# Kernel optimization log

Hardware: AMD Instinct MI355X
Metric: run time of the kernel (lower is better)

## Reference

```python
import jax, jax.numpy as jnp
import numpy as np

B, S, F, D = 64, 129, 768, 4
MOM = 0.9
EPS = 1e-6


def setup_inputs() -> dict:
    key = jax.random.key(0)
    ks = jax.random.split(key, 8)
    x = jax.random.normal(ks[0], (B, S, F), dtype=jnp.float32)
    labels = jax.random.randint(ks[1], (B,), 0, 16, dtype=jnp.int32)
    domain = jax.random.randint(ks[2], (B,), 0, D, dtype=jnp.int32)
    lmda = jax.random.beta(ks[3], 0.1, 0.1, (B, 1, 1)).astype(jnp.float32)
    d_rand = jax.random.randint(ks[4], (B,), 1, D, dtype=jnp.int32)  # range(1, num_domains)
    mean_buf = (0.1 * jax.random.normal(ks[5], (D, F))).astype(jnp.float32)
    var_buf = jax.random.uniform(ks[6], (D, F), minval=0.5, maxval=1.5, dtype=jnp.float32)
    hg_noise = jax.random.normal(ks[7], (B, S, F), dtype=jnp.float32)
    return {"input": x, "lmda": lmda, "mean_buf": mean_buf, "var_buf": var_buf,
            "hg_noise": hg_noise, "labels": labels, "domain": domain, "d_rand": d_rand}


def reference(input, lmda, mean_buf, var_buf, hg_noise, labels, domain, d_rand):
    x = input  # [B,S,F]
    b, s, f = x.shape
    d = mean_buf.shape[0]

    # --- per-domain mean/var over dims [0,1] (unbiased), momentum buffer update ---
    tok = x.reshape(b * s, f)
    seg = jnp.repeat(domain, s)  # [B*S]
    cnt = jax.ops.segment_sum(jnp.ones((b * s,), x.dtype), seg, num_segments=d)  # tokens/domain
    s1 = jax.ops.segment_sum(tok, seg, num_segments=d)          # [D,F]
    s2 = jax.ops.segment_sum(tok * tok, seg, num_segments=d)    # [D,F]
    n = cnt[:, None]
    mu_d = s1 / jnp.maximum(n, 1.0)
    var_d = (s2 - n * mu_d * mu_d) / jnp.maximum(n - 1.0, 1.0)  # unbiased, matches torch.var
    present = (cnt > 0)[:, None]
    new_mean = jnp.where(present, MOM * mean_buf + (1.0 - MOM) * mu_d, mean_buf)
    new_var = jnp.where(present, MOM * var_buf + (1.0 - MOM) * var_d, var_buf)

    # --- instance renorm over token dim (unbiased var) + cross-domain restyle ---
    mu_i = x.mean(1, keepdims=True)
    v_i = x.var(1, keepdims=True, ddof=1)
    x_normed = (x - mu_i) * jax.lax.rsqrt(v_i + EPS)
    ds = (domain + d_rand) % d
    x_new = x_normed * jnp.sqrt(new_var[ds] + EPS)[:, None, :] + new_mean[ds][:, None, :]
    x_mix = lmda * x + (1.0 - lmda) * x_new

    # --- Gaussian hallucinated samples from own-domain stats ---
    hg = new_mean[domain][:, None, :] + jnp.sqrt(new_var[domain] + EPS)[:, None, :] * hg_noise

    # --- pairwise euclidean distance + hard example mining + soft-margin triplet loss ---
    xe = jnp.concatenate([x, x_mix, hg], axis=0).reshape(3 * b, s * f)  # [3B, S*F]
    ln = jnp.concatenate([labels, labels, -jnp.ones((b,), labels.dtype)])
    sq = jnp.sum(xe * xe, axis=1)
    d2 = sq[:, None] + sq[None, :] - 2.0 * (xe @ xe.T)
    dist = jnp.sqrt(jnp.clip(d2, 1e-12))
    pos = ln[:, None] == ln[None, :]
    big = jnp.asarray(1e30, dist.dtype)
    dist_ap = jnp.max(jnp.where(pos, dist, -big), axis=1)
    dist_an = jnp.min(jnp.where(pos, big, dist), axis=1)
    tri_hard_loss = jnp.mean(jax.nn.softplus(dist_ap - dist_an))  # SoftMarginLoss, y=1

    return x_mix, tri_hard_loss, new_mean, new_var
```

## Files before the change

### kernel.cpp

```cpp
#include <hip/hip_runtime.h>
#include <math.h>

#define B_ 64
#define S_ 129
#define F_ 768
#define N3 192
#define BF 49152
#define NCHUNK 1548
#define GMAIN 256
#define GSZ 36864

#define WS_NM   0
#define WS_SV   3072
#define WS_C1   6144
#define WS_C0   55296
#define WS_HGM  104448
#define WS_HGS  153600
#define WS_S1   202752
#define WS_S2   251904
#define WS_PART 337920

#define OUT_LOSS 6340608
#define OUT_NM   6340609
#define OUT_NV   6343681

typedef unsigned int uint;
using short8v = __attribute__((ext_vector_type(8))) short;
using float4v = __attribute__((ext_vector_type(4))) float;

__global__ void k_stats(const float* __restrict__ x,
                        float* __restrict__ s1, float* __restrict__ s2) {
    __shared__ float4 r1[256], r2[256];
    int b = blockIdx.x / 3, fg = blockIdx.x % 3;
    int c = threadIdx.x & 63, sp = threadIdx.x >> 6;
    int f = fg * 256 + c * 4;
    const float* p = x + (size_t)b * S_ * F_ + f;
    int s0 = sp * 32;
    int se = s0 + 32 + (sp == 3 ? 1 : 0);
    float4 a1 = {0.f,0.f,0.f,0.f}, a2 = {0.f,0.f,0.f,0.f};
#pragma unroll 4
    for (int s = s0; s < se; ++s) {
        float4 v = *(const float4*)(p + s * F_);
        a1.x += v.x; a1.y += v.y; a1.z += v.z; a1.w += v.w;
        a2.x += v.x*v.x; a2.y += v.y*v.y; a2.z += v.z*v.z; a2.w += v.w*v.w;
    }
    r1[threadIdx.x] = a1; r2[threadIdx.x] = a2;
    __syncthreads();
    if (sp == 0) {
        float4 t1 = r1[c], t2 = r2[c];
#pragma unroll
        for (int k = 1; k < 4; ++k) {
            float4 u1 = r1[k * 64 + c], u2 = r2[k * 64 + c];
            t1.x += u1.x; t1.y += u1.y; t1.z += u1.z; t1.w += u1.w;
            t2.x += u2.x; t2.y += u2.y; t2.z += u2.z; t2.w += u2.w;
        }
        *(float4*)(s1 + b * F_ + f) = t1;
        *(float4*)(s2 + b * F_ + f) = t2;
    }
}

__global__ void k_dom(const float* __restrict__ s1, const float* __restrict__ s2,
                      const int* __restrict__ domain,
                      const float* __restrict__ mean_buf, const float* __restrict__ var_buf,
                      float* __restrict__ nm_tab, float* __restrict__ sv_tab,
                      float* __restrict__ out_nm, float* __restrict__ out_nv) {
    int idx = blockIdx.x * 256 + threadIdx.x;
    if (idx >= F_ * 4) return;
    int f = idx >> 2, d = idx & 3;
    float a1 = 0.f, a2 = 0.f, cntf = 0.f;
#pragma unroll 8
    for (int b = 0; b < B_; ++b) {
        float v1 = s1[b * F_ + f];
        float v2 = s2[b * F_ + f];
        bool mk = (domain[b] == d);
        a1 += mk ? v1 : 0.0f;
        a2 += mk ? v2 : 0.0f;
        cntf += mk ? 1.0f : 0.0f;
    }
    float nm, nv;
    if (cntf > 0.f) {
        float n = cntf * (float)S_;
        float mu = a1 / n;
        float var = (a2 - n * mu * mu) / fmaxf(n - 1.0f, 1.0f);
        nm = 0.9f * mean_buf[d * F_ + f] + 0.1f * mu;
        nv = 0.9f * var_buf[d * F_ + f] + 0.1f * var;
    } else {
        nm = mean_buf[d * F_ + f];
        nv = var_buf[d * F_ + f];
    }
    out_nm[d * F_ + f] = nm;
    out_nv[d * F_ + f] = nv;
    nm_tab[d * F_ + f] = nm;
    sv_tab[d * F_ + f] = sqrtf(nv + 1e-6f);
}

__global__ void k_coef(const float* __restrict__ s1, const float* __restrict__ s2,
                       const float* __restrict__ lmda,
                       const int* __restrict__ domain, const int* __restrict__ d_rand,
                       const float* __restrict__ nm_tab, const float* __restrict__ sv_tab,
                       float* __restrict__ c1, float* __restrict__ c0,
                       float* __restrict__ hgm, float* __restrict__ hgs,
                       float* __restrict__ out_loss) {
    int t = blockIdx.x * 256 + threadIdx.x;
    if (blockIdx.x == 0 && threadIdx.x == 0) out_loss[0] = 0.0f;
    int b = t / F_, f = t - b * F_;
    float mu = s1[t] * (1.0f / (float)S_);
    float v  = (s2[t] - (float)S_ * mu * mu) * (1.0f / (float)(S_ - 1));
    float r  = rsqrtf(v + 1e-6f);
    int dm = domain[b];
    int ds = (dm + d_rand[b]) & 3;
    float sv = sv_tab[ds * F_ + f];
    float nm = nm_tab[ds * F_ + f];
    float lam = lmda[b];
    float rs = r * sv;
    c1[t] = lam + (1.0f - lam) * rs;
    c0[t] = (1.0f - lam) * (nm - mu * rs);
    hgm[t] = nm_tab[dm * F_ + f];
    hgs[t] = sv_tab[dm * F_ + f];
}

__device__ __forceinline__ uint pack2(float a, float b) {
    uint ua = __float_as_uint(a);
    uint ub = __float_as_uint(b);
    uint ha = (ua + 0x7FFFu + ((ua >> 16) & 1u)) >> 16;
    uint hb = (ub + 0x7FFFu + ((ub >> 16) & 1u)) & 0xFFFF0000u;
    return hb | ha;
}

__device__ __forceinline__ void bf16_store8(char* lds, int row, int g,
                                            float4 v0, float4 v1) {
    uint4 H;
    H.x = pack2(v0.x, v0.y);
    H.y = pack2(v0.z, v0.w);
    H.z = pack2(v1.x, v1.y);
    H.w = pack2(v1.z, v1.w);
    *(uint4*)(lds + row * 128 + ((g ^ (row & 7)) << 4)) = H;
}

__device__ __forceinline__ float4 fma4(float4 a, float4 x, float4 b) {
    float4 r;
    r.x = fmaf(a.x, x.x, b.x); r.y = fmaf(a.y, x.y, b.y);
    r.z = fmaf(a.z, x.z, b.z); r.w = fmaf(a.w, x.w, b.w);
    return r;
}

template <bool EXCL>
__global__ __launch_bounds__(512, 2)
void k_main(const float* __restrict__ x, const float* __restrict__ hgn,
            const float* __restrict__ c1, const float* __restrict__ c0,
            const float* __restrict__ hgm, const float* __restrict__ hgs,
            float* __restrict__ xmix, float* part, int npart) {
    __shared__ __align__(16) char LDS[49152];
    float4v acc[6][3];
#pragma unroll
    for (int i = 0; i < 6; ++i)
#pragma unroll
        for (int j = 0; j < 3; ++j)
            acc[i][j] = (float4v){0.f, 0.f, 0.f, 0.f};

    int tid = threadIdx.x;
    int b = tid >> 3;
    int g = tid & 7;
    int w = tid >> 6;
    int wr = (w >> 2) * 96, wc = (w & 3) * 48;
    int lane = tid & 63, m = lane & 15, qd = lane >> 4;

    int q = blockIdx.x;
    size_t goff; int cb;
    {
        int s = q / 12, f0 = (q - s * 12) * 64;
        goff = ((size_t)b * S_ + s) * F_ + f0 + (g << 3);
        cb = b * F_ + f0 + (g << 3);
    }
    float4 X0 = ((const float4*)(x + goff))[0];
    float4 X1 = ((const float4*)(x + goff))[1];
    float4 N0 = ((const float4*)(hgn + goff))[0];
    float4 N1 = ((const float4*)(hgn + goff))[1];
    float4 C1a = ((const float4*)(c1 + cb))[0], C1b = ((const float4*)(c1 + cb))[1];
    float4 C0a = ((const float4*)(c0 + cb))[0], C0b = ((const float4*)(c0 + cb))[1];
    float4 HMa = ((const float4*)(hgm + cb))[0], HMb = ((const float4*)(hgm + cb))[1];
    float4 HSa = ((const float4*)(hgs + cb))[0], HSb = ((const float4*)(hgs + cb))[1];

    int par = 0;
    for (; q < NCHUNK; q += GMAIN) {
        char* buf = LDS + par * 24576;
        float4 M0 = fma4(C1a, X0, C0a);
        float4 M1 = fma4(C1b, X1, C0b);
        ((float4*)(xmix + goff))[0] = M0;
        ((float4*)(xmix + goff))[1] = M1;
        float4 H0 = fma4(HSa, N0, HMa);
        float4 H1 = fma4(HSb, N1, HMb);

        bf16_store8(buf, b, g, X0, X1);
        bf16_store8(buf, 64 + b, g, M0, M1);
        bf16_store8(buf, 128 + b, g, H0, H1);
        __syncthreads();

        int qn = q + GMAIN;
        if (qn < NCHUNK) {
            int s = qn / 12, f0 = (qn - s * 12) * 64;
            goff = ((size_t)b * S_ + s) * F_ + f0 + (g << 3);
            cb = b * F_ + f0 + (g << 3);
            X0 = ((const float4*)(x + goff))[0];
            X1 = ((const float4*)(x + goff))[1];
            N0 = ((const float4*)(hgn + goff))[0];
            N1 = ((const float4*)(hgn + goff))[1];
            C1a = ((const float4*)(c1 + cb))[0]; C1b = ((const float4*)(c1 + cb))[1];
            C0a = ((const float4*)(c0 + cb))[0]; C0b = ((const float4*)(c0 + cb))[1];
            HMa = ((const float4*)(hgm + cb))[0]; HMb = ((const float4*)(hgm + cb))[1];
            HSa = ((const float4*)(hgs + cb))[0]; HSb = ((const float4*)(hgs + cb))[1];
        }

#pragma unroll
        for (int t = 0; t < 2; ++t) {
            short8v A[6];
#pragma unroll
            for (int i = 0; i < 6; ++i) {
                int row = wr + i * 16 + m;
                int go = (((t << 2) + qd) ^ (row & 7)) << 4;
                A[i] = *(const short8v*)(buf + row * 128 + go);
            }
#pragma unroll
            for (int j = 0; j < 3; ++j) {
                int row = wc + j * 16 + m;
                int go = (((t << 2) + qd) ^ (row & 7)) << 4;
                short8v Bv = *(const short8v*)(buf + row * 128 + go);
#pragma unroll
                for (int i = 0; i < 6; ++i)
                    acc[i][j] = __builtin_amdgcn_mfma_f32_16x16x32_bf16(A[i], Bv, acc[i][j], 0, 0, 0);
            }
        }
        par ^= 1;
    }

    float* dst = part + (size_t)(blockIdx.x % npart) * GSZ;
#pragma unroll
    for (int i = 0; i < 6; ++i)
#pragma unroll
        for (int j = 0; j < 3; ++j) {
            int base = (wr + i * 16 + qd * 4) * N3 + wc + j * 16 + m;
#pragma unroll
            for (int r = 0; r < 4; ++r) {
                int o = base + r * N3;
                if (EXCL) dst[o] = acc[i][j][r];
                else atomicAdd(dst + o, acc[i][j][r]);
            }
        }
}

__global__ void k_red(const float* __restrict__ part, float* __restrict__ gram, int npart) {
    int j = blockIdx.x * 256 + threadIdx.x;
    float s = 0.0f;
#pragma unroll 8
    for (int p = 0; p < npart; ++p) s += part[(size_t)p * GSZ + j];
    gram[j] = s;
}

__global__ void k_loss(const float* __restrict__ gram, const int* __restrict__ labels,
                       float* __restrict__ out_loss) {
    __shared__ float sq[N3];
    __shared__ int ln[N3];
    int i = blockIdx.x, lane = threadIdx.x;
    for (int k = lane; k < N3; k += 64) {
        sq[k] = gram[k * (N3 + 1)];
        ln[k] = (k < 128) ? labels[k & 63] : -1;
    }
    __syncthreads();
    int li = ln[i];
    float si = sq[i];
    float ap = -1e30f, an = 1e30f;
    for (int j = lane; j < N3; j += 64) {
        float d2 = si + sq[j] - 2.0f * gram[i * N3 + j];
        float dist = sqrtf(fmaxf(d2, 1e-12f));
        bool pos = (li == ln[j]);
        ap = pos ? fmaxf(ap, dist) : ap;
        an = pos ? an : fminf(an, dist);
    }
#pragma unroll
    for (int off = 32; off; off >>= 1) {
        ap = fmaxf(ap, __shfl_xor(ap, off));
        an = fminf(an, __shfl_xor(an, off));
    }
    if (lane == 0) {
        float xv = ap - an;
        float sp = fmaxf(xv, 0.0f) + log1pf(expf(-fabsf(xv)));
        atomicAdd(out_loss, sp * (1.0f / (float)N3));
    }
}

extern "C" void kernel_launch(void* const* d_in, const int* in_sizes, int n_in,
                              void* d_out, int out_size, void* d_ws, size_t ws_size,
                              hipStream_t stream) {
    const float* x        = (const float*)d_in[0];
    const float* lmda     = (const float*)d_in[1];
    const float* mean_buf = (const float*)d_in[2];
    const float* var_buf  = (const float*)d_in[3];
    const float* hgn      = (const float*)d_in[4];
    const int*   labels   = (const int*)d_in[5];
    const int*   domain   = (const int*)d_in[6];
    const int*   d_rand   = (const int*)d_in[7];
    float* out = (float*)d_out;
    float* ws  = (float*)d_ws;

    long avail = (long)(ws_size / 4) - WS_PART;
    int npart = (int)(avail / GSZ) - 1;
    if (npart < 1) npart = 1;
    if (npart > GMAIN) npart = GMAIN;
    bool excl = (npart == GMAIN);
    float* part = ws + WS_PART;
    float* gram = ws + WS_PART + (size_t)npart * GSZ;

    k_stats<<<dim3(192), dim3(256), 0, stream>>>(x, ws + WS_S1, ws + WS_S2);
    k_dom<<<dim3(12), dim3(256), 0, stream>>>(ws + WS_S1, ws + WS_S2, domain,
                                              mean_buf, var_buf,
                                              ws + WS_NM, ws + WS_SV,
                                              out + OUT_NM, out + OUT_NV);
    k_coef<<<dim3(192), dim3(256), 0, stream>>>(ws + WS_S1, ws + WS_S2, lmda,
                                                domain, d_rand,
                                                ws + WS_NM, ws + WS_SV,
                                                ws + WS_C1, ws + WS_C0,
                                                ws + WS_HGM, ws + WS_HGS,
                                                out + OUT_LOSS);
    if (!excl) {
        hipMemsetAsync(part, 0, (size_t)npart * GSZ * 4, stream);
    }
    if (excl) {
        k_main<true><<<dim3(GMAIN), dim3(512), 0, stream>>>(
            x, hgn, ws + WS_C1, ws + WS_C0, ws + WS_HGM, ws + WS_HGS,
            out, part, npart);
    } else {
        k_main<false><<<dim3(GMAIN), dim3(512), 0, stream>>>(
            x, hgn, ws + WS_C1, ws + WS_C0, ws + WS_HGM, ws + WS_HGS,
            out, part, npart);
    }
    k_red<<<dim3(144), dim3(256), 0, stream>>>(part, gram, npart);
    k_loss<<<dim3(N3), dim3(64), 0, stream>>>(gram, labels, out + OUT_LOSS);
}
```

Before: 160.7 us.

## Prefetch x/noise two chunks ahead and fuse gram reduction with loss kernel

The main Gram kernel now keeps two register sets for x and noise, loading each chunk two iterations ahead, while the per-chunk coefficients are still loaded one ahead. This aims to hide more global-load latency behind the MFMA work. The separate partial-sum reduction and loss kernels are merged into one kernel that reduces each Gram row directly. That kernel reads the diagonal from a small per-slice array that k_main writes alongside the partials, which removes one launch and the intermediate Gram round trip. The cost is higher register pressure in the main loop, plus 192 blocks that each do a strided sum over all partial slices.

```diff
diff --git a/kernel.cpp b/kernel.cpp
--- a/kernel.cpp
+++ b/kernel.cpp
@@ -144,12 +144,76 @@
     return r;
 }
 
+__device__ __forceinline__ void chunk_body(
+    int q, char* buf,
+    float4& X0, float4& X1, float4& N0, float4& N1, size_t& goff,
+    float4& C1a, float4& C1b, float4& C0a, float4& C0b,
+    float4& HMa, float4& HMb, float4& HSa, float4& HSb,
+    const float* __restrict__ x, const float* __restrict__ hgn,
+    const float* __restrict__ c1, const float* __restrict__ c0,
+    const float* __restrict__ hgm, const float* __restrict__ hgs,
+    float* __restrict__ xmix,
+    int b, int g, int wr, int wc, int m, int qd,
+    float4v (&acc)[6][3])
+{
+    float4 M0 = fma4(C1a, X0, C0a);
+    float4 M1 = fma4(C1b, X1, C0b);
+    ((float4*)(xmix + goff))[0] = M0;
+    ((float4*)(xmix + goff))[1] = M1;
+    float4 H0 = fma4(HSa, N0, HMa);
+    float4 H1 = fma4(HSb, N1, HMb);
+
+    bf16_store8(buf, b, g, X0, X1);
+    bf16_store8(buf, 64 + b, g, M0, M1);
+    bf16_store8(buf, 128 + b, g, H0, H1);
+    __syncthreads();
+
+    int q1 = q + GMAIN;
+    if (q1 < NCHUNK) {
+        int s = q1 / 12, f0 = (q1 - s * 12) * 64;
+        int cb = b * F_ + f0 + (g << 3);
+        C1a = ((const float4*)(c1 + cb))[0]; C1b = ((const float4*)(c1 + cb))[1];
+        C0a = ((const float4*)(c0 + cb))[0]; C0b = ((const float4*)(c0 + cb))[1];
+        HMa = ((const float4*)(hgm + cb))[0]; HMb = ((const float4*)(hgm + cb))[1];
+        HSa = ((const float4*)(hgs + cb))[0]; HSb = ((const float4*)(hgs + cb))[1];
+    }
+    int q2 = q + 2 * GMAIN;
+    if (q2 < NCHUNK) {
+        int s = q2 / 12, f0 = (q2 - s * 12) * 64;
+        goff = ((size_t)b * S_ + s) * F_ + f0 + (g << 3);
+        X0 = ((const float4*)(x + goff))[0];
+        X1 = ((const float4*)(x + goff))[1];
+        N0 = ((const float4*)(hgn + goff))[0];
+        N1 = ((const float4*)(hgn + goff))[1];
+    }
+
+#pragma unroll
+    for (int t = 0; t < 2; ++t) {
+        short8v A[6];
+#pragma unroll
+        for (int i = 0; i < 6; ++i) {
+            int row = wr + i * 16 + m;
+            int go = (((t << 2) + qd) ^ (row & 7)) << 4;
+            A[i] = *(const short8v*)(buf + row * 128 + go);
+        }
+#pragma unroll
+        for (int j = 0; j < 3; ++j) {
+            int row = wc + j * 16 + m;
+            int go = (((t << 2) + qd) ^ (row & 7)) << 4;
+            short8v Bv = *(const short8v*)(buf + row * 128 + go);
+#pragma unroll
+            for (int i = 0; i < 6; ++i)
+                acc[i][j] = __builtin_amdgcn_mfma_f32_16x16x32_bf16(A[i], Bv, acc[i][j], 0, 0, 0);
+        }
+    }
+}
+
 template <bool EXCL>
 __global__ __launch_bounds__(512, 2)
 void k_main(const float* __restrict__ x, const float* __restrict__ hgn,
             const float* __restrict__ c1, const float* __restrict__ c0,
             const float* __restrict__ hgm, const float* __restrict__ hgs,
-            float* __restrict__ xmix, float* part, int npart) {
+            float* __restrict__ xmix, float* part, float* diag, int npart) {
     __shared__ __align__(16) char LDS[49152];
     float4v acc[6][3];
 #pragma unroll
@@ -165,124 +229,116 @@
     int wr = (w >> 2) * 96, wc = (w & 3) * 48;
     int lane = tid & 63, m = lane & 15, qd = lane >> 4;
 
-    int q = blockIdx.x;
-    size_t goff; int cb;
+    int q0 = blockIdx.x;
+    size_t goA, goB;
+    float4 XA0, XA1, NA0, NA1, XB0, XB1, NB0, NB1;
+    float4 C1a, C1b, C0a, C0b, HMa, HMb, HSa, HSb;
     {
-        int s = q / 12, f0 = (q - s * 12) * 64;
-        goff = ((size_t)b * S_ + s) * F_ + f0 + (g << 3);
-        cb = b * F_ + f0 + (g << 3);
-    }
-    float4 X0 = ((const float4*)(x + goff))[0];
-    float4 X1 = ((const float4*)(x + goff))[1];
-    float4 N0 = ((const float4*)(hgn + goff))[0];
-    float4 N1 = ((const float4*)(hgn + goff))[1];
-    float4 C1a = ((const float4*)(c1 + cb))[0], C1b = ((const float4*)(c1 + cb))[1];
-    float4 C0a = ((const float4*)(c0 + cb))[0], C0b = ((const float4*)(c0 + cb))[1];
-    float4 HMa = ((const float4*)(hgm + cb))[0], HMb = ((const float4*)(hgm + cb))[1];
-    float4 HSa = ((const float4*)(hgs + cb))[0], HSb = ((const float4*)(hgs + cb))[1];
+        int s = q0 / 12, f0 = (q0 - s * 12) * 64;
+        goA = ((size_t)b * S_ + s) * F_ + f0 + (g << 3);
+        int cb = b * F_ + f0 + (g << 3);
+        XA0 = ((const float4*)(x + goA))[0];
+        XA1 = ((const float4*)(x + goA))[1];
+        NA0 = ((const float4*)(hgn + goA))[0];
+        NA1 = ((const float4*)(hgn + goA))[1];
+        C1a = ((const float4*)(c1 + cb))[0]; C1b = ((const float4*)(c1 + cb))[1];
+        C0a = ((const float4*)(c0 + cb))[0]; C0b = ((const float4*)(c0 + cb))[1];
+        HMa = ((const float4*)(hgm + cb))[0]; HMb = ((const float4*)(hgm + cb))[1];
+        HSa = ((const float4*)(hgs + cb))[0]; HSb = ((const float4*)(hgs + cb))[1];
+    }
+    {
+        int q1 = q0 + GMAIN;
+        int s = q1 / 12, f0 = (q1 - s * 12) * 64;
+        goB = ((size_t)b * S_ + s) * F_ + f0 + (g << 3);
+        XB0 = ((const float4*)(x + goB))[0];
+        XB1 = ((const float4*)(x + goB))[1];
+        NB0 = ((const float4*)(hgn + goB))[0];
+        NB1 = ((const float4*)(hgn + goB))[1];
+    }
 
     int par = 0;
-    for (; q < NCHUNK; q += GMAIN) {
-        char* buf = LDS + par * 24576;
-        float4 M0 = fma4(C1a, X0, C0a);
-        float4 M1 = fma4(C1b, X1, C0b);
-        ((float4*)(xmix + goff))[0] = M0;
-        ((float4*)(xmix + goff))[1] = M1;
-        float4 H0 = fma4(HSa, N0, HMa);
-        float4 H1 = fma4(HSb, N1, HMb);
-
-        bf16_store8(buf, b, g, X0, X1);
-        bf16_store8(buf, 64 + b, g, M0, M1);
-        bf16_store8(buf, 128 + b, g, H0, H1);
-        __syncthreads();
-
-        int qn = q + GMAIN;
-        if (qn < NCHUNK) {
-            int s = qn / 12, f0 = (qn - s * 12) * 64;
-            goff = ((size_t)b * S_ + s) * F_ + f0 + (g << 3);
-            cb = b * F_ + f0 + (g << 3);
-            X0 = ((const float4*)(x + goff))[0];
-            X1 = ((const float4*)(x + goff))[1];
-            N0 = ((const float4*)(hgn + goff))[0];
-            N1 = ((const float4*)(hgn + goff))[1];
-            C1a = ((const float4*)(c1 + cb))[0]; C1b = ((const float4*)(c1 + cb))[1];
-            C0a = ((const float4*)(c0 + cb))[0]; C0b = ((const float4*)(c0 + cb))[1];
-            HMa = ((const float4*)(hgm + cb))[0]; HMb = ((const float4*)(hgm + cb))[1];
-            HSa = ((const float4*)(hgs + cb))[0]; HSb = ((const float4*)(hgs + cb))[1];
-        }
-
-#pragma unroll
-        for (int t = 0; t < 2; ++t) {
-            short8v A[6];
-#pragma unroll
-            for (int i = 0; i < 6; ++i) {
-                int row = wr + i * 16 + m;
-                int go = (((t << 2) + qd) ^ (row & 7)) << 4;
-                A[i] = *(const short8v*)(buf + row * 128 + go);
+    for (int q = q0; q < NCHUNK; q += GMAIN, par ^= 1) {
+        if (par == 0)
+            chunk_body(q, LDS, XA0, XA1, NA0, NA1, goA,
+                       C1a, C1b, C0a, C0b, HMa, HMb, HSa, HSb,
+                       x, hgn, c1, c0, hgm, hgs, xmix, b, g, wr, wc, m, qd, acc);
+        else
+            chunk_body(q, LDS + 24576, XB0, XB1, NB0, NB1, goB,
+                       C1a, C1b, C0a, C0b, HMa, HMb, HSa, HSb,
+                       x, hgn, c1, c0, hgm, hgs, xmix, b, g, wr, wc, m, qd, acc);
+    }
+
+    int slice = blockIdx.x % npart;
+    float* dst  = part + (size_t)slice * GSZ;
+    float* dstd = diag + (size_t)slice * N3;
+#pragma unroll
+    for (int i = 0; i < 6; ++i)
+#pragma unroll
+        for (int j = 0; j < 3; ++j) {
+            int col = wc + j * 16 + m;
+#pragma unroll
+            for (int r = 0; r < 4; ++r) {
+                int row = wr + i * 16 + qd * 4 + r;
+                int o = row * N3 + col;
+                float v = acc[i][j][r];
+                if (EXCL) {
+                    dst[o] = v;
+                    if (row == col) dstd[row] = v;
+                } else {
+                    atomicAdd(dst + o, v);
+                    if (row == col) atomicAdd(dstd + row, v);
+                }
             }
-#pragma unroll
-            for (int j = 0; j < 3; ++j) {
-                int row = wc + j * 16 + m;
-                int go = (((t << 2) + qd) ^ (row & 7)) << 4;
-                short8v Bv = *(const short8v*)(buf + row * 128 + go);
-#pragma unroll
-                for (int i = 0; i < 6; ++i)
-                    acc[i][j] = __builtin_amdgcn_mfma_f32_16x16x32_bf16(A[i], Bv, acc[i][j], 0, 0, 0);
-            }
-        }
-        par ^= 1;
-    }
-
-    float* dst = part + (size_t)(blockIdx.x % npart) * GSZ;
-#pragma unroll
-    for (int i = 0; i < 6; ++i)
-#pragma unroll
-        for (int j = 0; j < 3; ++j) {
-            int base = (wr + i * 16 + qd * 4) * N3 + wc + j * 16 + m;
-#pragma unroll
-            for (int r = 0; r < 4; ++r) {
-                int o = base + r * N3;
-                if (EXCL) dst[o] = acc[i][j][r];
-                else atomicAdd(dst + o, acc[i][j][r]);
-            }
-        }
-}
-
-__global__ void k_red(const float* __restrict__ part, float* __restrict__ gram, int npart) {
-    int j = blockIdx.x * 256 + threadIdx.x;
-    float s = 0.0f;
-#pragma unroll 8
-    for (int p = 0; p < npart; ++p) s += part[(size_t)p * GSZ + j];
-    gram[j] = s;
-}
-
-__global__ void k_loss(const float* __restrict__ gram, const int* __restrict__ labels,
-                       float* __restrict__ out_loss) {
-    __shared__ float sq[N3];
-    __shared__ int ln[N3];
-    int i = blockIdx.x, lane = threadIdx.x;
-    for (int k = lane; k < N3; k += 64) {
-        sq[k] = gram[k * (N3 + 1)];
-        ln[k] = (k < 128) ? labels[k & 63] : -1;
+        }
+}
+
+__global__ void k_redloss(const float* __restrict__ part, const float* __restrict__ diag,
+                          const int* __restrict__ labels, float* __restrict__ out_loss,
+                          int npart) {
+    __shared__ float sqs[N3];
+    __shared__ float apw[4], anw[4];
+    int i = blockIdx.x, j = threadIdx.x;
+    float rowv = 0.f, dv = 0.f;
+    if (j < N3) {
+        const float* pr = part + (size_t)i * N3 + j;
+        const float* pd = diag + j;
+        int p = 0;
+        for (; p + 4 <= npart; p += 4) {
+            rowv += pr[(size_t)(p + 0) * GSZ] + pr[(size_t)(p + 1) * GSZ]
+                  + pr[(size_t)(p + 2) * GSZ] + pr[(size_t)(p + 3) * GSZ];
+            dv   += pd[(p + 0) * N3] + pd[(p + 1) * N3]
+                  + pd[(p + 2) * N3] + pd[(p + 3) * N3];
+        }
+        for (; p < npart; ++p) {
+            rowv += pr[(size_t)p * GSZ];
+            dv   += pd[p * N3];
+        }
+        sqs[j] = dv;
     }
     __syncthreads();
-    int li = ln[i];
-    float si = sq[i];
+    float si = sqs[i];
     float ap = -1e30f, an = 1e30f;
-    for (int j = lane; j < N3; j += 64) {
-        float d2 = si + sq[j] - 2.0f * gram[i * N3 + j];
+    if (j < N3) {
+        int li = (i < 128) ? labels[i & 63] : -1;
+        int lj = (j < 128) ? labels[j & 63] : -1;
+        float d2 = si + sqs[j] - 2.0f * rowv;
         float dist = sqrtf(fmaxf(d2, 1e-12f));
-        bool pos = (li == ln[j]);
-        ap = pos ? fmaxf(ap, dist) : ap;
-        an = pos ? an : fminf(an, dist);
+        bool pos = (li == lj);
+        ap = pos ? dist : -1e30f;
+        an = pos ? 1e30f : dist;
     }
 #pragma unroll
     for (int off = 32; off; off >>= 1) {
         ap = fmaxf(ap, __shfl_xor(ap, off));
         an = fminf(an, __shfl_xor(an, off));
     }
-    if (lane == 0) {
-        float xv = ap - an;
+    int wv = j >> 6;
+    if ((j & 63) == 0) { apw[wv] = ap; anw[wv] = an; }
+    __syncthreads();
+    if (j == 0) {
+        float a = fmaxf(fmaxf(apw[0], apw[1]), fmaxf(apw[2], apw[3]));
+        float n = fminf(fminf(anw[0], anw[1]), fminf(anw[2], anw[3]));
+        float xv = a - n;
         float sp = fmaxf(xv, 0.0f) + log1pf(expf(-fabsf(xv)));
         atomicAdd(out_loss, sp * (1.0f / (float)N3));
     }
@@ -303,12 +359,12 @@
     float* ws  = (float*)d_ws;
 
     long avail = (long)(ws_size / 4) - WS_PART;
-    int npart = (int)(avail / GSZ) - 1;
+    int npart = (int)(avail / (GSZ + N3));
     if (npart < 1) npart = 1;
     if (npart > GMAIN) npart = GMAIN;
     bool excl = (npart == GMAIN);
     float* part = ws + WS_PART;
-    float* gram = ws + WS_PART + (size_t)npart * GSZ;
+    float* diag = part + (size_t)npart * GSZ;
 
     k_stats<<<dim3(192), dim3(256), 0, stream>>>(x, ws + WS_S1, ws + WS_S2);
     k_dom<<<dim3(12), dim3(256), 0, stream>>>(ws + WS_S1, ws + WS_S2, domain,
@@ -322,17 +378,17 @@
                                                 ws + WS_HGM, ws + WS_HGS,
                                                 out + OUT_LOSS);
     if (!excl) {
-        hipMemsetAsync(part, 0, (size_t)npart * GSZ * 4, stream);
+        hipMemsetAsync(part, 0, (size_t)npart * (GSZ + N3) * 4, stream);
     }
     if (excl) {
         k_main<true><<<dim3(GMAIN), dim3(512), 0, stream>>>(
             x, hgn, ws + WS_C1, ws + WS_C0, ws + WS_HGM, ws + WS_HGS,
-            out, part, npart);
+            out, part, diag, npart);
     } else {
         k_main<false><<<dim3(GMAIN), dim3(512), 0, stream>>>(
             x, hgn, ws + WS_C1, ws + WS_C0, ws + WS_HGM, ws + WS_HGS,
-            out, part, npart);
-    }
-    k_red<<<dim3(144), dim3(256), 0, stream>>>(part, gram, npart);
-    k_loss<<<dim3(N3), dim3(64), 0, stream>>>(gram, labels, out + OUT_LOSS);
-}
+            out, part, diag, npart);
+    }
+    k_redloss<<<dim3(N3), dim3(256), 0, stream>>>(part, diag, labels,
+                                                  out + OUT_LOSS, npart);
+}
```

Result: slower. 206.6 us (+28.5%).
